# Performance work log

Measured on AMD Instinct MI355X. Metric: run time of the kernel, lower is better.

The kernel has to match this reference:

```python
import jax, jax.numpy as jnp
import numpy as np


def conv2d(x, w, b):
    pad = (w.shape[-1] - 1) // 2
    y = jax.lax.conv_general_dilated(x, w, (1, 1), [(pad, pad), (pad, pad)],
                                     dimension_numbers=('NCHW', 'OIHW', 'NCHW'))
    return y + b[None, :, None, None]


def mish(x):
    return x * jnp.tanh(jax.nn.softplus(x))


def setup_inputs() -> dict:
    key = jax.random.key(0)
    ks = jax.random.split(key, 8)
    B, C, H, W = 8, 16, 256, 256
    s = 0.1
    return dict(
        x=jax.random.normal(ks[0], (B, C, H, W), jnp.float32),
        W1=jax.random.normal(ks[1], (4, 1, 3, 3), jnp.float32) * s,      # conv1: 1->4, k=3
        b1=jnp.zeros((4,), jnp.float32),
        Wred=jax.random.normal(ks[2], (1, 4, 1, 1), jnp.float32) * s,    # involution reduce 4->1
        bred=jnp.zeros((1,), jnp.float32),
        Wspan=jax.random.normal(ks[3], (9, 1, 1, 1), jnp.float32) * s,   # involution span 1->k^2
        bspan=jnp.zeros((9,), jnp.float32),
        W2=jax.random.normal(ks[4], (C, 4 * C, 3, 3), jnp.float32) * s,  # conv2: 4C->C, k=3
        b2=jnp.zeros((C,), jnp.float32),
        Weca=jax.random.normal(ks[5], (3,), jnp.float32) * s,            # ECA 1D conv kernel
    )


def reference(x, W1, b1, Wred, bred, Wspan, bspan, W2, b2, Weca):
    B, C, H, W = x.shape
    H2 = H // 2
    K2 = 9  # 3x3 involution kernel
    # per-channel 1->4 conv + Mish: vectorize the Python channel loop by folding C into batch
    xs = x.reshape(B * C, 1, H, W)
    f = mish(conv2d(xs, W1, b1))                      # (B*C, 4, H, W)
    top, bot = f[:, :, :H2], f[:, :, H2:]             # each (B*C, 4, H2, W)
    # involution2(y1, y2): dynamic per-pixel 3x3 kernel from bottom half, applied to top half
    ker = conv2d(jax.nn.relu(conv2d(bot, Wred, bred)), Wspan, bspan)   # (B*C, 9, H2, W)
    patches = jax.lax.conv_general_dilated_patches(
        top, (3, 3), (1, 1), [(1, 1), (1, 1)],
        dimension_numbers=('NCHW', 'OIHW', 'NCHW'))                    # (B*C, 4*9, H2, W), channel-major
    patches = patches.reshape(B * C, 4, K2, H2, W)
    top_inv = (patches * ker[:, None]).sum(axis=2)                     # (B*C, 4, H2, W)
    # shuffle/concat: out channel-block i = [inv_top_i ; bottom_{(i+1) % C}] along height
    ti = top_inv.reshape(B, C, 4, H2, W)
    bo = bot.reshape(B, C, 4, H2, W)
    shuffled = jnp.concatenate([ti, jnp.roll(bo, -1, axis=1)], axis=3)  # (B, C, 4, H, W)
    shuffled = shuffled.reshape(B, 4 * C, H, W)
    out = mish(conv2d(shuffled, W2, b2))               # (B, C, H, W)
    # ECA: gate from global-avg-pooled `out`, 1D cross-correlation (k=3, pad=1) over channels
    pooled = out.mean(axis=(2, 3))                     # (B, C)
    yp = jnp.pad(pooled, ((0, 0), (1, 1)))
    gate = jax.nn.sigmoid(Weca[0] * yp[:, :-2] + Weca[1] * yp[:, 1:-1] + Weca[2] * yp[:, 2:])
    return x * gate[:, :, None, None]
```

## Files before the change

kernel.cpp:

```cpp
#include <hip/hip_runtime.h>
#include <hip/hip_bf16.h>

#define H 256
#define Wd 256
#define H2 128

typedef unsigned short ushort_t;
typedef __attribute__((ext_vector_type(8))) short short8;
typedef __attribute__((ext_vector_type(4))) float f32x4;
typedef __attribute__((ext_vector_type(2))) float f32x2;

__device__ __forceinline__ float mishf(float v){
  if (v > 15.f) return v;
  float e = __expf(v);
  float w = e*(e+2.f);
  return v * w * __builtin_amdgcn_rcpf(w + 2.f);
}

__device__ __forceinline__ ushort_t f2bf(float f){
  unsigned int u = __float_as_uint(f);
  u += 0x7fffu + ((u >> 16) & 1u);
  return (ushort_t)(u >> 16);
}
__device__ __forceinline__ float bf2f(ushort_t h){
  return __uint_as_float(((unsigned int)h) << 16);
}
__device__ __forceinline__ unsigned packbf(float a, float b){
  return (unsigned)f2bf(a) | ((unsigned)f2bf(b) << 16);
}
__device__ __forceinline__ float lo16(unsigned u){
  return __uint_as_float(u << 16);
}
__device__ __forceinline__ float hi16(unsigned u){
  return __uint_as_float(u & 0xffff0000u);
}


__global__ void k0_pack(const float* __restrict__ W2, ushort_t* __restrict__ wpack)
{
  int idx = blockIdx.x*128 + threadIdx.x;
  if (idx >= 1152) return;
  int lane  = idx & 63;
  int s     = (idx >> 6) % 9;
  int khalf = idx / 576;
  int n = lane & 15, g = lane >> 4;
  unsigned int w[4];
#pragma unroll
  for (int h = 0; h < 4; ++h){
    int ch0 = khalf*32 + g*8 + 2*h;
    unsigned lo = f2bf(W2[(n*64 + ch0  )*9 + s]);
    unsigned hi = f2bf(W2[(n*64 + ch0+1)*9 + s]);
    w[h] = lo | (hi << 16);
  }
  *(uint4*)(wpack + (size_t)idx*8) = make_uint4(w[0], w[1], w[2], w[3]);
}

__global__ __launch_bounds__(256) void k12(
    const float* __restrict__ x, const float* __restrict__ W1,
    const float* __restrict__ b1, const float* __restrict__ Wred,
    const float* __restrict__ bred, const float* __restrict__ Wspan,
    const float* __restrict__ bspan, ushort_t* __restrict__ shuf)
{
  __shared__ float xt[20][73];
  __shared__ float xb[18][73];
  __shared__ unsigned ftp[2][18][69];

  int bid = blockIdx.x;
  int n   = bid >> 5;
  int t   = bid & 31;
  int itop0 = (t >> 2) * 16;
  int j0    = (t & 3) * 64;
  int tid = threadIdx.x;
  const float* xp = x + (size_t)n * (H*Wd);

  f32x2 w01[9], w23[9], b01, b23, wspb[9];
  float wredr[4];
  float bredr = bred[0];
#pragma unroll
  for (int k=0;k<9;k++){
    w01[k] = f32x2{W1[k], W1[9+k]};
    w23[k] = f32x2{W1[18+k], W1[27+k]};
    wspb[k] = f32x2{Wspan[k], bspan[k]};
  }
  b01 = f32x2{b1[0], b1[1]};
  b23 = f32x2{b1[2], b1[3]};
#pragma unroll
  for (int m=0;m<4;m++) wredr[m] = Wred[m];

  for (int idx=tid; idx<360; idx+=256){
    int r = idx/18, q = idx - r*18;
    int grow = itop0-2+r, gcol = j0-4+q*4;
    float4 v = make_float4(0.f,0.f,0.f,0.f);
    if (grow>=0 && gcol>=0 && gcol<Wd)
      v = *(const float4*)(xp + (size_t)grow*Wd + gcol);
    int c0 = q*4;
    xt[r][c0] = v.x; xt[r][c0+1] = v.y; xt[r][c0+2] = v.z; xt[r][c0+3] = v.w;
  }
  for (int idx=tid; idx<324; idx+=256){
    int r = idx/18, q = idx - r*18;
    int grow = 127+itop0+r, gcol = j0-4+q*4;
    float4 v = make_float4(0.f,0.f,0.f,0.f);
    if (grow<H && gcol>=0 && gcol<Wd)
      v = *(const float4*)(xp + (size_t)grow*Wd + gcol);
    int c0 = q*4;
    xb[r][c0] = v.x; xb[r][c0+1] = v.y; xb[r][c0+2] = v.z; xb[r][c0+3] = v.w;
  }
  __syncthreads();

  for (int idx=tid; idx<18*66; idx+=256){
    int r = idx/66, c = idx - r*66;
    int frow = itop0-1+r, fcol = j0-1+c;
    unsigned u01 = 0u, u23 = 0u;
    if (frow>=0 && frow<H2 && fcol>=0 && fcol<Wd){
      f32x2 s01 = b01, s23 = b23;
#pragma unroll
      for (int ky=0;ky<3;ky++)
#pragma unroll
        for (int kx=0;kx<3;kx++){
          float xv = xt[r+ky][c+kx+2];
          f32x2 xv2 = f32x2{xv, xv};
          s01 = xv2*w01[ky*3+kx] + s01;
          s23 = xv2*w23[ky*3+kx] + s23;
        }
      u01 = packbf(mishf(s01.x), mishf(s01.y));
      u23 = packbf(mishf(s23.x), mishf(s23.y));
    }
    ftp[0][r][c] = u01;
    ftp[1][r][c] = u23;
  }

  int lr  = tid >> 4;
  int lc4 = (tid & 15) * 4;
  int trow = itop0 + lr;
  int bq = n >> 4, cq = n & 15;

  float fb[4][4];
  {
    float xv[3][6];
#pragma unroll
    for (int r=0;r<3;r++)
#pragma unroll
      for (int c=0;c<6;c++)
        xv[r][c] = xb[lr+r][lc4+3+c];
#pragma unroll
    for (int p=0;p<4;p++){
      f32x2 s01 = b01, s23 = b23;
#pragma unroll
      for (int ky=0;ky<3;ky++)
#pragma unroll
        for (int kx=0;kx<3;kx++){
          float v = xv[ky][p+kx];
          f32x2 v2 = f32x2{v, v};
          s01 = v2*w01[ky*3+kx] + s01;
          s23 = v2*w23[ky*3+kx] + s23;
        }
      fb[0][p] = mishf(s01.x); fb[1][p] = mishf(s01.y);
      fb[2][p] = mishf(s23.x); fb[3][p] = mishf(s23.y);
    }
  }
  int cdst = (cq + 15) & 15;
  size_t bbase = ((size_t)(bq*16 + cdst))*65536 + (size_t)(128+trow)*256 + j0 + lc4;
  {
    unsigned w0 = packbf(fb[0][0], fb[1][0]), w1 = packbf(fb[2][0], fb[3][0]);
    unsigned w2 = packbf(fb[0][1], fb[1][1]), w3 = packbf(fb[2][1], fb[3][1]);
    *(uint4*)(shuf + bbase*4) = make_uint4(w0,w1,w2,w3);
    unsigned w4 = packbf(fb[0][2], fb[1][2]), w5 = packbf(fb[2][2], fb[3][2]);
    unsigned w6 = packbf(fb[0][3], fb[1][3]), w7 = packbf(fb[2][3], fb[3][3]);
    *(uint4*)(shuf + (bbase+2)*4) = make_uint4(w4,w5,w6,w7);
  }
  float gv[4];
#pragma unroll
  for (int p=0;p<4;p++){
    float s = bredr;
#pragma unroll
    for (int m=0;m<4;m++) s = fmaf(fb[m][p], wredr[m], s);
    gv[p] = fmaxf(s, 0.f);
  }

  __syncthreads();

  unsigned fv0[3][6], fv1[3][6];
#pragma unroll
  for (int ky=0;ky<3;ky++)
#pragma unroll
    for (int c=0;c<6;c++){
      fv0[ky][c] = ftp[0][lr+ky][lc4+c];
      fv1[ky][c] = ftp[1][lr+ky][lc4+c];
    }

  float o[4][4];
#pragma unroll
  for (int p=0;p<4;p++){
    f32x2 ab0 = f32x2{0.f,0.f}, ab1 = ab0, ab2 = ab0, ab3 = ab0;
#pragma unroll
    for (int ky=0;ky<3;ky++)
#pragma unroll
      for (int kx=0;kx<3;kx++){
        f32x2 w = wspb[ky*3+kx];
        unsigned u0 = fv0[ky][p+kx], u1 = fv1[ky][p+kx];
        float a = lo16(u0), b = hi16(u0), c2 = lo16(u1), d = hi16(u1);
        ab0 = f32x2{a,a}*w + ab0;
        ab1 = f32x2{b,b}*w + ab1;
        ab2 = f32x2{c2,c2}*w + ab2;
        ab3 = f32x2{d,d}*w + ab3;
      }
    o[0][p] = fmaf(gv[p], ab0.x, ab0.y);
    o[1][p] = fmaf(gv[p], ab1.x, ab1.y);
    o[2][p] = fmaf(gv[p], ab2.x, ab2.y);
    o[3][p] = fmaf(gv[p], ab3.x, ab3.y);
  }
  size_t pbase = ((size_t)(bq*16 + cq))*65536 + (size_t)trow*256 + j0 + lc4;
  {
    unsigned w0 = packbf(o[0][0], o[1][0]), w1 = packbf(o[2][0], o[3][0]);
    unsigned w2 = packbf(o[0][1], o[1][1]), w3 = packbf(o[2][1], o[3][1]);
    *(uint4*)(shuf + pbase*4) = make_uint4(w0,w1,w2,w3);
    unsigned w4 = packbf(o[0][2], o[1][2]), w5 = packbf(o[2][2], o[3][2]);
    unsigned w6 = packbf(o[0][3], o[1][3]), w7 = packbf(o[2][3], o[3][3]);
    *(uint4*)(shuf + (pbase+2)*4) = make_uint4(w4,w5,w6,w7);
  }
}

__global__ __launch_bounds__(256) void k3_conv2(
    const ushort_t* __restrict__ shuf, const ushort_t* __restrict__ wpack,
    const float* __restrict__ b2, float* __restrict__ scratch)
{
  __shared__ f32x4 mg[2][8][64];
  __shared__ float pacc[16];

  int bid0 = blockIdx.x;
  int bid  = (bid0 & 7)*256 + (bid0 >> 3);
  int b   = bid >> 8;
  int t   = bid & 255;
  int rb  = t >> 3;
  int cb  = t & 7;
  int tid = threadIdx.x;
  int lane = tid & 63;
  int n = lane & 15;
  int g = lane >> 4;
  int wid = tid >> 6;
  int colhalf = wid & 1;
  int khalf   = wid >> 1;

  if (tid < 16) pacc[tid] = 0.f;

  const short8* wp = (const short8*)wpack + (size_t)khalf*576 + lane;
  short8 afr[9];
#pragma unroll
  for (int s = 0; s < 9; ++s) afr[s] = wp[s*64];

  f32x4 acc[8];
#pragma unroll
  for (int r = 0; r < 8; ++r) acc[r] = f32x4{0.f,0.f,0.f,0.f};

  int r0 = rb*8 - 1;
  int c  = cb*32 - 1 + colhalf*16 + n;
  int p0 = khalf*8 + g*2;
  const ushort_t* sp = shuf + ((size_t)(b*16 + p0))*262144;

#pragma unroll
  for (int hr = 0; hr < 10; ++hr){
    int grow = r0 + hr;
    bool rok = (unsigned)grow < 256u;
    uint2 va[3], vb[3];
#pragma unroll
    for (int kx = 0; kx < 3; ++kx){
      int gcol = c + kx;
      uint2 a = make_uint2(0u,0u), bv = make_uint2(0u,0u);
      if (rok && (unsigned)gcol < 256u){
        const ushort_t* pp = sp + (size_t)(grow*256 + gcol)*4;
        a  = *(const uint2*)pp;
        bv = *(const uint2*)(pp + 262144);
      }
      va[kx] = a; vb[kx] = bv;
    }
#pragma unroll
    for (int kx = 0; kx < 3; ++kx){
      union { uint4 u; short8 s; } cv;
      cv.u = make_uint4(va[kx].x, va[kx].y, vb[kx].x, vb[kx].y);
#pragma unroll
      for (int ky = 0; ky < 3; ++ky){
        int orow = hr - ky;
        if (orow >= 0 && orow < 8){
          acc[orow] = __builtin_amdgcn_mfma_f32_16x16x32_bf16(
              afr[ky*3+kx], cv.s, acc[orow], 0, 0, 0);
        }
      }
    }
  }

  if (khalf == 1){
#pragma unroll
    for (int r = 0; r < 8; ++r) mg[colhalf][r][lane] = acc[r];
  }
  __syncthreads();

  if (khalf == 0){
    float b2v[4];
#pragma unroll
    for (int q = 0; q < 4; ++q) b2v[q] = b2[g*4 + q];
    float po[4] = {0.f, 0.f, 0.f, 0.f};
#pragma unroll
    for (int r = 0; r < 8; ++r){
      f32x4 o = acc[r] + mg[colhalf][r][lane];
#pragma unroll
      for (int q = 0; q < 4; ++q) po[q] += mishf(o[q] + b2v[q]);
    }
#pragma unroll
    for (int q = 0; q < 4; ++q){
#pragma unroll
      for (int mk = 1; mk < 16; mk <<= 1) po[q] += __shfl_xor(po[q], mk);
    }
    if (n == 0){
#pragma unroll
      for (int q = 0; q < 4; ++q) atomicAdd(&pacc[g*4 + q], po[q]);
    }
  }
  __syncthreads();
  if (tid < 16) scratch[bid*16 + tid] = pacc[tid];
}

__global__ void k4_gate(const float* __restrict__ scratch,
                        const float* __restrict__ Weca,
                        float* __restrict__ gate)
{
  __shared__ float rr[16][16];
  __shared__ float pool[16];
  int b = blockIdx.x;
  int t = threadIdx.x;
  int oc = t & 15, ch = t >> 4;
  float s = 0.f;
  for (int u = 0; u < 16; ++u)
    s += scratch[(size_t)(b*256 + ch*16 + u)*16 + oc];
  rr[ch][oc] = s;
  __syncthreads();
  if (t < 16){
    float tot = 0.f;
#pragma unroll
    for (int k = 0; k < 16; ++k) tot += rr[k][t];
    pool[t] = tot * (1.0f/65536.0f);
  }
  __syncthreads();
  if (t < 16){
    float pm = (t > 0)  ? pool[t-1] : 0.f;
    float p0 = pool[t];
    float pp = (t < 15) ? pool[t+1] : 0.f;
    float z = Weca[0]*pm + Weca[1]*p0 + Weca[2]*pp;
    gate[b*16 + t] = 1.f/(1.f + __expf(-z));
  }
}

__global__ __launch_bounds__(256) void k5_scale(
    const f32x4* __restrict__ x4, const float* __restrict__ gate,
    f32x4* __restrict__ out4)
{
  int idx = blockIdx.x*256 + threadIdx.x;
  float g = gate[idx >> 14];
  f32x4 v = x4[idx] * g;
  __builtin_nontemporal_store(v, &out4[idx]);
}

extern "C" void kernel_launch(void* const* d_in, const int* in_sizes, int n_in,
                              void* d_out, int out_size, void* d_ws, size_t ws_size,
                              hipStream_t stream)
{
  const float* x     = (const float*)d_in[0];
  const float* W1    = (const float*)d_in[1];
  const float* b1    = (const float*)d_in[2];
  const float* Wred  = (const float*)d_in[3];
  const float* bred  = (const float*)d_in[4];
  const float* Wspan = (const float*)d_in[5];
  const float* bspan = (const float*)d_in[6];
  const float* W2    = (const float*)d_in[7];
  const float* b2    = (const float*)d_in[8];
  const float* Weca  = (const float*)d_in[9];

  ushort_t* shuf    = (ushort_t*)d_ws;
  float*    gate    = (float*)((char*)d_ws + 67108864);
  ushort_t* wpack   = (ushort_t*)((char*)d_ws + 67108864 + 1024);
  float*    scratch = (float*)d_out;

  k0_pack<<<9, 128, 0, stream>>>(W2, wpack);
  k12    <<<4096, 256, 0, stream>>>(x, W1, b1, Wred, bred, Wspan, bspan, shuf);
  k3_conv2<<<2048, 256, 0, stream>>>(shuf, wpack, b2, scratch);
  k4_gate<<<8, 256, 0, stream>>>(scratch, Weca, gate);
  k5_scale<<<8192, 256, 0, stream>>>((const f32x4*)x, gate, (f32x4*)d_out);
}
```

Measured before the change: 85.45 us.

## Rewrite conv1+involution kernel as register-only row stencil with packed FMA asm

The fused conv1/Mish/involution kernel drops its shared-memory tiles and barriers. Each thread now loads its input rows straight from global memory and recomputes the top-half features in registers for each of the three involution rows. The span reduction is accumulated on the fly, and inline v_pk_fma_f32 asm with op_sel broadcasts does the 4-channel conv. This removes LDS traffic and syncs and keeps the top features in fp32 instead of bf16. The cost is about three times the conv1 and Mish recompute, more global loads per thread, and higher register pressure.

```diff
diff --git a/kernel.cpp b/kernel.cpp
--- a/kernel.cpp
+++ b/kernel.cpp
@@ -28,12 +28,13 @@
 __device__ __forceinline__ unsigned packbf(float a, float b){
   return (unsigned)f2bf(a) | ((unsigned)f2bf(b) << 16);
 }
-__device__ __forceinline__ float lo16(unsigned u){
-  return __uint_as_float(u << 16);
-}
-__device__ __forceinline__ float hi16(unsigned u){
-  return __uint_as_float(u & 0xffff0000u);
-}
+
+#define PK_LO(acc, f, w) \
+  asm("v_pk_fma_f32 %0, %1, %2, %0 op_sel_hi:[1,0,1]" \
+      : "+v"(acc) : "v"(f), "s"(w))
+#define PK_HI(acc, f, w) \
+  asm("v_pk_fma_f32 %0, %1, %2, %0 op_sel:[0,1,0] op_sel_hi:[1,1,1]" \
+      : "+v"(acc) : "v"(f), "s"(w))
 
 
 __global__ void k0_pack(const float* __restrict__ W2, ushort_t* __restrict__ wpack)
@@ -55,111 +56,131 @@
   *(uint4*)(wpack + (size_t)idx*8) = make_uint4(w[0], w[1], w[2], w[3]);
 }
 
-__global__ __launch_bounds__(256) void k12(
+__global__ __launch_bounds__(256) void k12r(
     const float* __restrict__ x, const float* __restrict__ W1,
     const float* __restrict__ b1, const float* __restrict__ Wred,
     const float* __restrict__ bred, const float* __restrict__ Wspan,
     const float* __restrict__ bspan, ushort_t* __restrict__ shuf)
 {
-  __shared__ float xt[20][73];
-  __shared__ float xb[18][73];
-  __shared__ unsigned ftp[2][18][69];
-
   int bid = blockIdx.x;
   int n   = bid >> 5;
-  int t   = bid & 31;
-  int itop0 = (t >> 2) * 16;
-  int j0    = (t & 3) * 64;
+  int rg  = bid & 31;
   int tid = threadIdx.x;
+  int i   = rg*4 + (tid >> 6);
+  int j0  = (tid & 63) * 4;
   const float* xp = x + (size_t)n * (H*Wd);
-
-  f32x2 w01[9], w23[9], b01, b23, wspb[9];
-  float wredr[4];
+  bool jlo = (j0 == 0), jhi = (j0 == 252);
+
+  f32x2 w01[9], w23[9];
+  float wsp[9], bsp[9], wredr[4];
   float bredr = bred[0];
 #pragma unroll
   for (int k=0;k<9;k++){
     w01[k] = f32x2{W1[k], W1[9+k]};
     w23[k] = f32x2{W1[18+k], W1[27+k]};
-    wspb[k] = f32x2{Wspan[k], bspan[k]};
-  }
-  b01 = f32x2{b1[0], b1[1]};
-  b23 = f32x2{b1[2], b1[3]};
+    wsp[k] = Wspan[k]; bsp[k] = bspan[k];
+  }
 #pragma unroll
   for (int m=0;m<4;m++) wredr[m] = Wred[m];
-
-  for (int idx=tid; idx<360; idx+=256){
-    int r = idx/18, q = idx - r*18;
-    int grow = itop0-2+r, gcol = j0-4+q*4;
-    float4 v = make_float4(0.f,0.f,0.f,0.f);
-    if (grow>=0 && gcol>=0 && gcol<Wd)
-      v = *(const float4*)(xp + (size_t)grow*Wd + gcol);
-    int c0 = q*4;
-    xt[r][c0] = v.x; xt[r][c0+1] = v.y; xt[r][c0+2] = v.z; xt[r][c0+3] = v.w;
-  }
-  for (int idx=tid; idx<324; idx+=256){
-    int r = idx/18, q = idx - r*18;
-    int grow = 127+itop0+r, gcol = j0-4+q*4;
-    float4 v = make_float4(0.f,0.f,0.f,0.f);
-    if (grow<H && gcol>=0 && gcol<Wd)
-      v = *(const float4*)(xp + (size_t)grow*Wd + gcol);
-    int c0 = q*4;
-    xb[r][c0] = v.x; xb[r][c0+1] = v.y; xb[r][c0+2] = v.z; xb[r][c0+3] = v.w;
-  }
-  __syncthreads();
-
-  for (int idx=tid; idx<18*66; idx+=256){
-    int r = idx/66, c = idx - r*66;
-    int frow = itop0-1+r, fcol = j0-1+c;
-    unsigned u01 = 0u, u23 = 0u;
-    if (frow>=0 && frow<H2 && fcol>=0 && fcol<Wd){
-      f32x2 s01 = b01, s23 = b23;
-#pragma unroll
-      for (int ky=0;ky<3;ky++)
-#pragma unroll
-        for (int kx=0;kx<3;kx++){
-          float xv = xt[r+ky][c+kx+2];
-          f32x2 xv2 = f32x2{xv, xv};
-          s01 = xv2*w01[ky*3+kx] + s01;
-          s23 = xv2*w23[ky*3+kx] + s23;
-        }
-      u01 = packbf(mishf(s01.x), mishf(s01.y));
-      u23 = packbf(mishf(s23.x), mishf(s23.y));
-    }
-    ftp[0][r][c] = u01;
-    ftp[1][r][c] = u23;
-  }
-
-  int lr  = tid >> 4;
-  int lc4 = (tid & 15) * 4;
-  int trow = itop0 + lr;
+  f32x2 bp0 = f32x2{b1[0], b1[0]};
+  f32x2 bp1 = f32x2{b1[1], b1[1]};
+  f32x2 bp2 = f32x2{b1[2], b1[2]};
+  f32x2 bp3 = f32x2{b1[3], b1[3]};
+
+  const float4 f4z = make_float4(0.f,0.f,0.f,0.f);
+  f32x2 PA[7], PB[7], PC[7];
+
+#define LROWP(row_, P_) { \
+    int row__ = (row_); \
+    float4 lm=f4z, mm=f4z, rm=f4z; \
+    if ((unsigned)row__ < 256u){ \
+      const float* rp = xp + (size_t)row__*Wd + j0; \
+      mm = *(const float4*)rp; \
+      if (!jlo) lm = *(const float4*)(rp-4); \
+      if (!jhi) rm = *(const float4*)(rp+4); \
+    } \
+    P_[0] = f32x2{lm.z, lm.w}; \
+    P_[1] = f32x2{lm.w, mm.x}; \
+    P_[2] = f32x2{mm.x, mm.y}; \
+    P_[3] = f32x2{mm.y, mm.z}; \
+    P_[4] = f32x2{mm.z, mm.w}; \
+    P_[5] = f32x2{mm.w, rm.x}; \
+    P_[6] = f32x2{rm.x, rm.y}; \
+  }
+
+  float A[4][4], Bv[4][4];
+#pragma unroll
+  for (int m=0;m<4;m++)
+#pragma unroll
+    for (int p=0;p<4;p++){ A[m][p]=0.f; Bv[m][p]=0.f; }
+
+#define CONVSPAN(R0_, R1_, R2_, KY_) { \
+    float fm[4][6]; \
+    _Pragma("unroll") \
+    for (int cp=0; cp<3; ++cp){ \
+      f32x2 s0=bp0, s1=bp1, s2=bp2, s3=bp3; \
+      _Pragma("unroll") \
+      for (int kx=0; kx<3; ++kx){ \
+        PK_LO(s0, R0_[2*cp+kx], w01[kx]);   PK_HI(s1, R0_[2*cp+kx], w01[kx]); \
+        PK_LO(s2, R0_[2*cp+kx], w23[kx]);   PK_HI(s3, R0_[2*cp+kx], w23[kx]); \
+        PK_LO(s0, R1_[2*cp+kx], w01[3+kx]); PK_HI(s1, R1_[2*cp+kx], w01[3+kx]); \
+        PK_LO(s2, R1_[2*cp+kx], w23[3+kx]); PK_HI(s3, R1_[2*cp+kx], w23[3+kx]); \
+        PK_LO(s0, R2_[2*cp+kx], w01[6+kx]); PK_HI(s1, R2_[2*cp+kx], w01[6+kx]); \
+        PK_LO(s2, R2_[2*cp+kx], w23[6+kx]); PK_HI(s3, R2_[2*cp+kx], w23[6+kx]); \
+      } \
+      fm[0][2*cp]=mishf(s0.x); fm[0][2*cp+1]=mishf(s0.y); \
+      fm[1][2*cp]=mishf(s1.x); fm[1][2*cp+1]=mishf(s1.y); \
+      fm[2][2*cp]=mishf(s2.x); fm[2][2*cp+1]=mishf(s2.y); \
+      fm[3][2*cp]=mishf(s3.x); fm[3][2*cp+1]=mishf(s3.y); \
+    } \
+    if (jlo){ fm[0][0]=0.f; fm[1][0]=0.f; fm[2][0]=0.f; fm[3][0]=0.f; } \
+    if (jhi){ fm[0][5]=0.f; fm[1][5]=0.f; fm[2][5]=0.f; fm[3][5]=0.f; } \
+    _Pragma("unroll") \
+    for (int m=0;m<4;m++) \
+      _Pragma("unroll") \
+      for (int p=0;p<4;p++){ \
+        _Pragma("unroll") \
+        for (int kx=0;kx<3;kx++){ \
+          A[m][p]  = fmaf(fm[m][p+kx], wsp[(KY_)*3+kx], A[m][p]); \
+          Bv[m][p] = fmaf(fm[m][p+kx], bsp[(KY_)*3+kx], Bv[m][p]); \
+        } \
+      } \
+  }
+
+  LROWP(i-2, PA); LROWP(i-1, PB); LROWP(i, PC);
+  if (i >= 1) { CONVSPAN(PA, PB, PC, 0); }
+  LROWP(i+1, PA);
+  { CONVSPAN(PB, PC, PA, 1); }
+  LROWP(i+2, PB);
+  if (i <= 126) { CONVSPAN(PC, PA, PB, 2); }
+
+  LROWP(127+i, PA); LROWP(128+i, PB); LROWP(129+i, PC);
+  f32x2 sA0=bp0,sA1=bp1,sA2=bp2,sA3=bp3;
+  f32x2 sB0=bp0,sB1=bp1,sB2=bp2,sB3=bp3;
+#pragma unroll
+  for (int kx=0; kx<3; ++kx){
+    PK_LO(sA0, PA[1+kx], w01[kx]);   PK_HI(sA1, PA[1+kx], w01[kx]);
+    PK_LO(sA2, PA[1+kx], w23[kx]);   PK_HI(sA3, PA[1+kx], w23[kx]);
+    PK_LO(sB0, PA[3+kx], w01[kx]);   PK_HI(sB1, PA[3+kx], w01[kx]);
+    PK_LO(sB2, PA[3+kx], w23[kx]);   PK_HI(sB3, PA[3+kx], w23[kx]);
+    PK_LO(sA0, PB[1+kx], w01[3+kx]); PK_HI(sA1, PB[1+kx], w01[3+kx]);
+    PK_LO(sA2, PB[1+kx], w23[3+kx]); PK_HI(sA3, PB[1+kx], w23[3+kx]);
+    PK_LO(sB0, PB[3+kx], w01[3+kx]); PK_HI(sB1, PB[3+kx], w01[3+kx]);
+    PK_LO(sB2, PB[3+kx], w23[3+kx]); PK_HI(sB3, PB[3+kx], w23[3+kx]);
+    PK_LO(sA0, PC[1+kx], w01[6+kx]); PK_HI(sA1, PC[1+kx], w01[6+kx]);
+    PK_LO(sA2, PC[1+kx], w23[6+kx]); PK_HI(sA3, PC[1+kx], w23[6+kx]);
+    PK_LO(sB0, PC[3+kx], w01[6+kx]); PK_HI(sB1, PC[3+kx], w01[6+kx]);
+    PK_LO(sB2, PC[3+kx], w23[6+kx]); PK_HI(sB3, PC[3+kx], w23[6+kx]);
+  }
+  float fb[4][4];
+  fb[0][0]=mishf(sA0.x); fb[0][1]=mishf(sA0.y); fb[0][2]=mishf(sB0.x); fb[0][3]=mishf(sB0.y);
+  fb[1][0]=mishf(sA1.x); fb[1][1]=mishf(sA1.y); fb[1][2]=mishf(sB1.x); fb[1][3]=mishf(sB1.y);
+  fb[2][0]=mishf(sA2.x); fb[2][1]=mishf(sA2.y); fb[2][2]=mishf(sB2.x); fb[2][3]=mishf(sB2.y);
+  fb[3][0]=mishf(sA3.x); fb[3][1]=mishf(sA3.y); fb[3][2]=mishf(sB3.x); fb[3][3]=mishf(sB3.y);
+
   int bq = n >> 4, cq = n & 15;
-
-  float fb[4][4];
-  {
-    float xv[3][6];
-#pragma unroll
-    for (int r=0;r<3;r++)
-#pragma unroll
-      for (int c=0;c<6;c++)
-        xv[r][c] = xb[lr+r][lc4+3+c];
-#pragma unroll
-    for (int p=0;p<4;p++){
-      f32x2 s01 = b01, s23 = b23;
-#pragma unroll
-      for (int ky=0;ky<3;ky++)
-#pragma unroll
-        for (int kx=0;kx<3;kx++){
-          float v = xv[ky][p+kx];
-          f32x2 v2 = f32x2{v, v};
-          s01 = v2*w01[ky*3+kx] + s01;
-          s23 = v2*w23[ky*3+kx] + s23;
-        }
-      fb[0][p] = mishf(s01.x); fb[1][p] = mishf(s01.y);
-      fb[2][p] = mishf(s23.x); fb[3][p] = mishf(s23.y);
-    }
-  }
   int cdst = (cq + 15) & 15;
-  size_t bbase = ((size_t)(bq*16 + cdst))*65536 + (size_t)(128+trow)*256 + j0 + lc4;
+  size_t bbase = ((size_t)(bq*16 + cdst))*65536 + (size_t)(128+i)*256 + j0;
   {
     unsigned w0 = packbf(fb[0][0], fb[1][0]), w1 = packbf(fb[2][0], fb[3][0]);
     unsigned w2 = packbf(fb[0][1], fb[1][1]), w3 = packbf(fb[2][1], fb[3][1]);
@@ -177,39 +198,14 @@
     gv[p] = fmaxf(s, 0.f);
   }
 
-  __syncthreads();
-
-  unsigned fv0[3][6], fv1[3][6];
-#pragma unroll
-  for (int ky=0;ky<3;ky++)
-#pragma unroll
-    for (int c=0;c<6;c++){
-      fv0[ky][c] = ftp[0][lr+ky][lc4+c];
-      fv1[ky][c] = ftp[1][lr+ky][lc4+c];
-    }
-
   float o[4][4];
 #pragma unroll
-  for (int p=0;p<4;p++){
-    f32x2 ab0 = f32x2{0.f,0.f}, ab1 = ab0, ab2 = ab0, ab3 = ab0;
-#pragma unroll
-    for (int ky=0;ky<3;ky++)
-#pragma unroll
-      for (int kx=0;kx<3;kx++){
-        f32x2 w = wspb[ky*3+kx];
-        unsigned u0 = fv0[ky][p+kx], u1 = fv1[ky][p+kx];
-        float a = lo16(u0), b = hi16(u0), c2 = lo16(u1), d = hi16(u1);
-        ab0 = f32x2{a,a}*w + ab0;
-        ab1 = f32x2{b,b}*w + ab1;
-        ab2 = f32x2{c2,c2}*w + ab2;
-        ab3 = f32x2{d,d}*w + ab3;
-      }
-    o[0][p] = fmaf(gv[p], ab0.x, ab0.y);
-    o[1][p] = fmaf(gv[p], ab1.x, ab1.y);
-    o[2][p] = fmaf(gv[p], ab2.x, ab2.y);
-    o[3][p] = fmaf(gv[p], ab3.x, ab3.y);
-  }
-  size_t pbase = ((size_t)(bq*16 + cq))*65536 + (size_t)trow*256 + j0 + lc4;
+  for (int m=0;m<4;m++)
+#pragma unroll
+    for (int p=0;p<4;p++)
+      o[m][p] = fmaf(gv[p], A[m][p], Bv[m][p]);
+
+  size_t pbase = ((size_t)n)*65536 + (size_t)i*256 + j0;
   {
     unsigned w0 = packbf(o[0][0], o[1][0]), w1 = packbf(o[2][0], o[3][0]);
     unsigned w2 = packbf(o[0][1], o[1][1]), w3 = packbf(o[2][1], o[3][1]);
@@ -218,6 +214,8 @@
     unsigned w6 = packbf(o[0][3], o[1][3]), w7 = packbf(o[2][3], o[3][3]);
     *(uint4*)(shuf + (pbase+2)*4) = make_uint4(w4,w5,w6,w7);
   }
+#undef LROWP
+#undef CONVSPAN
 }
 
 __global__ __launch_bounds__(256) void k3_conv2(
@@ -380,7 +378,7 @@
   float*    scratch = (float*)d_out;
 
   k0_pack<<<9, 128, 0, stream>>>(W2, wpack);
-  k12    <<<4096, 256, 0, stream>>>(x, W1, b1, Wred, bred, Wspan, bspan, shuf);
+  k12r   <<<4096, 256, 0, stream>>>(x, W1, b1, Wred, bred, Wspan, bspan, shuf);
   k3_conv2<<<2048, 256, 0, stream>>>(shuf, wpack, b2, scratch);
   k4_gate<<<8, 256, 0, stream>>>(scratch, Weca, gate);
   k5_scale<<<8192, 256, 0, stream>>>((const f32x4*)x, gate, (f32x4*)d_out);
```

Measured after the change: 102.8 us. +20.3%, slower.

## Restructure conv1/involution kernel to read x directly and use packed LDS layout

Applied to the files above, without the earlier changes.

The fused conv1+mish+involution kernel no longer stages x tiles in shared memory. Each thread loads its 3x8 input window from global memory and computes 4 adjacent outputs for all 4 channels, then writes them as interleaved bf16 into a single LDS buffer read back with 16-byte vector loads. This removes a barrier and the LDS round-trip for x, and the mish overflow branch is dropped. The cost is redundant global reads, which rely on cache for reuse, plus higher register pressure. Dropping the overflow branch also risks inf/NaN from __expf on large inputs.

```diff
diff --git a/kernel.cpp b/kernel.cpp
--- a/kernel.cpp
+++ b/kernel.cpp
@@ -8,7 +8,6 @@
 typedef unsigned short ushort_t;
 typedef __attribute__((ext_vector_type(8))) short short8;
 typedef __attribute__((ext_vector_type(4))) float f32x4;
-typedef __attribute__((ext_vector_type(2))) float f32x2;
 
 __device__ __forceinline__ float mishf(float v){
   if (v > 15.f) return v;
@@ -16,14 +15,16 @@
   float w = e*(e+2.f);
   return v * w * __builtin_amdgcn_rcpf(w + 2.f);
 }
+__device__ __forceinline__ float mish_s(float v){
+  float e = __expf(v);
+  float w = e*(e+2.f);
+  return v * w * __builtin_amdgcn_rcpf(w + 2.f);
+}
 
 __device__ __forceinline__ ushort_t f2bf(float f){
   unsigned int u = __float_as_uint(f);
   u += 0x7fffu + ((u >> 16) & 1u);
   return (ushort_t)(u >> 16);
-}
-__device__ __forceinline__ float bf2f(ushort_t h){
-  return __uint_as_float(((unsigned int)h) << 16);
 }
 __device__ __forceinline__ unsigned packbf(float a, float b){
   return (unsigned)f2bf(a) | ((unsigned)f2bf(b) << 16);
@@ -55,15 +56,14 @@
   *(uint4*)(wpack + (size_t)idx*8) = make_uint4(w[0], w[1], w[2], w[3]);
 }
 
-__global__ __launch_bounds__(256) void k12(
+#define FT_STRIDE 560
+__global__ __launch_bounds__(256) void k12h(
     const float* __restrict__ x, const float* __restrict__ W1,
     const float* __restrict__ b1, const float* __restrict__ Wred,
     const float* __restrict__ bred, const float* __restrict__ Wspan,
     const float* __restrict__ bspan, ushort_t* __restrict__ shuf)
 {
-  __shared__ float xt[20][73];
-  __shared__ float xb[18][73];
-  __shared__ unsigned ftp[2][18][69];
+  __shared__ __align__(16) char ftl[18*FT_STRIDE];
 
   int bid = blockIdx.x;
   int n   = bid >> 5;
@@ -72,94 +72,106 @@
   int j0    = (t & 3) * 64;
   int tid = threadIdx.x;
   const float* xp = x + (size_t)n * (H*Wd);
-
-  f32x2 w01[9], w23[9], b01, b23, wspb[9];
-  float wredr[4];
+  const float4 f4z = make_float4(0.f,0.f,0.f,0.f);
+
+  float w1r[36], b1r[4], wsp[9], bsp[9], wredr[4];
   float bredr = bred[0];
 #pragma unroll
-  for (int k=0;k<9;k++){
-    w01[k] = f32x2{W1[k], W1[9+k]};
-    w23[k] = f32x2{W1[18+k], W1[27+k]};
-    wspb[k] = f32x2{Wspan[k], bspan[k]};
-  }
-  b01 = f32x2{b1[0], b1[1]};
-  b23 = f32x2{b1[2], b1[3]};
-#pragma unroll
-  for (int m=0;m<4;m++) wredr[m] = Wred[m];
-
-  for (int idx=tid; idx<360; idx+=256){
-    int r = idx/18, q = idx - r*18;
-    int grow = itop0-2+r, gcol = j0-4+q*4;
-    float4 v = make_float4(0.f,0.f,0.f,0.f);
-    if (grow>=0 && gcol>=0 && gcol<Wd)
-      v = *(const float4*)(xp + (size_t)grow*Wd + gcol);
-    int c0 = q*4;
-    xt[r][c0] = v.x; xt[r][c0+1] = v.y; xt[r][c0+2] = v.z; xt[r][c0+3] = v.w;
-  }
-  for (int idx=tid; idx<324; idx+=256){
-    int r = idx/18, q = idx - r*18;
-    int grow = 127+itop0+r, gcol = j0-4+q*4;
-    float4 v = make_float4(0.f,0.f,0.f,0.f);
-    if (grow<H && gcol>=0 && gcol<Wd)
-      v = *(const float4*)(xp + (size_t)grow*Wd + gcol);
-    int c0 = q*4;
-    xb[r][c0] = v.x; xb[r][c0+1] = v.y; xb[r][c0+2] = v.z; xb[r][c0+3] = v.w;
-  }
-  __syncthreads();
-
-  for (int idx=tid; idx<18*66; idx+=256){
-    int r = idx/66, c = idx - r*66;
-    int frow = itop0-1+r, fcol = j0-1+c;
-    unsigned u01 = 0u, u23 = 0u;
-    if (frow>=0 && frow<H2 && fcol>=0 && fcol<Wd){
-      f32x2 s01 = b01, s23 = b23;
-#pragma unroll
-      for (int ky=0;ky<3;ky++)
-#pragma unroll
-        for (int kx=0;kx<3;kx++){
-          float xv = xt[r+ky][c+kx+2];
-          f32x2 xv2 = f32x2{xv, xv};
-          s01 = xv2*w01[ky*3+kx] + s01;
-          s23 = xv2*w23[ky*3+kx] + s23;
+  for (int k=0;k<36;k++) w1r[k] = W1[k];
+#pragma unroll
+  for (int m=0;m<4;m++){ b1r[m] = b1[m]; wredr[m] = Wred[m]; }
+#pragma unroll
+  for (int k=0;k<9;k++){ wsp[k] = Wspan[k]; bsp[k] = bspan[k]; }
+
+#pragma unroll
+  for (int pi0 = 0; pi0 < 2; ++pi0){
+    int pi = tid + pi0*256;
+    if (pi < 306){
+      int r  = pi / 17;
+      int q  = pi - r*17;
+      int frow  = itop0 - 1 + r;
+      int fcol0 = j0 - 2 + 4*q;
+      uint4 o0 = make_uint4(0u,0u,0u,0u), o1 = make_uint4(0u,0u,0u,0u);
+      if ((unsigned)frow < 128u){
+        float v[3][8];
+        int cA = fcol0 - 2, cB = fcol0 + 2;
+#pragma unroll
+        for (int rr=0; rr<3; ++rr){
+          int xr = frow - 1 + rr;
+          bool rok = (xr >= 0);
+          const float* rp = xp + (size_t)xr*Wd;
+          float4 a = (rok && cA >= 0)   ? *(const float4*)(rp + cA) : f4z;
+          float4 b = (rok && cB <= 252) ? *(const float4*)(rp + cB) : f4z;
+          v[rr][0]=a.x; v[rr][1]=a.y; v[rr][2]=a.z; v[rr][3]=a.w;
+          v[rr][4]=b.x; v[rr][5]=b.y; v[rr][6]=b.z; v[rr][7]=b.w;
         }
-      u01 = packbf(mishf(s01.x), mishf(s01.y));
-      u23 = packbf(mishf(s23.x), mishf(s23.y));
-    }
-    ftp[0][r][c] = u01;
-    ftp[1][r][c] = u23;
+        float s[4][4];
+#pragma unroll
+        for (int m=0;m<4;m++)
+#pragma unroll
+          for (int p=0;p<4;p++) s[m][p] = b1r[m];
+#pragma unroll
+        for (int ky=0;ky<3;ky++)
+#pragma unroll
+          for (int kx=0;kx<3;kx++){
+#pragma unroll
+            for (int m=0;m<4;m++){
+              float wv = w1r[m*9+ky*3+kx];
+#pragma unroll
+              for (int p=0;p<4;p++)
+                s[m][p] = fmaf(v[ky][p+1+kx], wv, s[m][p]);
+            }
+          }
+        unsigned pw[8];
+#pragma unroll
+        for (int p=0;p<4;p++){
+          bool ok = (unsigned)(fcol0+p) < 256u;
+          pw[p*2]   = ok ? packbf(mish_s(s[0][p]), mish_s(s[1][p])) : 0u;
+          pw[p*2+1] = ok ? packbf(mish_s(s[2][p]), mish_s(s[3][p])) : 0u;
+        }
+        o0 = make_uint4(pw[0],pw[1],pw[2],pw[3]);
+        o1 = make_uint4(pw[4],pw[5],pw[6],pw[7]);
+      }
+      char* dst = ftl + r*FT_STRIDE + q*32;
+      *(uint4*)dst = o0;
+      *(uint4*)(dst+16) = o1;
+    }
   }
 
   int lr  = tid >> 4;
   int lc4 = (tid & 15) * 4;
   int trow = itop0 + lr;
   int bq = n >> 4, cq = n & 15;
-
+  int jc = j0 + lc4;
+
+  float vb[3][6];
+  bool look = (jc >= 4);
+  bool hiok = (jc <= 248);
+#pragma unroll
+  for (int rr=0; rr<3; ++rr){
+    int xr = 127 + trow + rr;
+    bool rok = (xr < 256);
+    const float* rp = xp + (size_t)xr*Wd + jc;
+    float4 m = rok ? *(const float4*)rp : f4z;
+    float lw = (rok && look) ? rp[-1] : 0.f;
+    float rw = (rok && hiok) ? rp[4]  : 0.f;
+    vb[rr][0]=lw; vb[rr][1]=m.x; vb[rr][2]=m.y; vb[rr][3]=m.z; vb[rr][4]=m.w; vb[rr][5]=rw;
+  }
   float fb[4][4];
-  {
-    float xv[3][6];
-#pragma unroll
-    for (int r=0;r<3;r++)
-#pragma unroll
-      for (int c=0;c<6;c++)
-        xv[r][c] = xb[lr+r][lc4+3+c];
+#pragma unroll
+  for (int m=0;m<4;m++)
 #pragma unroll
     for (int p=0;p<4;p++){
-      f32x2 s01 = b01, s23 = b23;
+      float s = b1r[m];
 #pragma unroll
       for (int ky=0;ky<3;ky++)
 #pragma unroll
-        for (int kx=0;kx<3;kx++){
-          float v = xv[ky][p+kx];
-          f32x2 v2 = f32x2{v, v};
-          s01 = v2*w01[ky*3+kx] + s01;
-          s23 = v2*w23[ky*3+kx] + s23;
-        }
-      fb[0][p] = mishf(s01.x); fb[1][p] = mishf(s01.y);
-      fb[2][p] = mishf(s23.x); fb[3][p] = mishf(s23.y);
-    }
-  }
+        for (int kx=0;kx<3;kx++)
+          s = fmaf(vb[ky][p+kx], w1r[m*9+ky*3+kx], s);
+      fb[m][p] = mish_s(s);
+    }
   int cdst = (cq + 15) & 15;
-  size_t bbase = ((size_t)(bq*16 + cdst))*65536 + (size_t)(128+trow)*256 + j0 + lc4;
+  size_t bbase = ((size_t)(bq*16 + cdst))*65536 + (size_t)(128+trow)*256 + jc;
   {
     unsigned w0 = packbf(fb[0][0], fb[1][0]), w1 = packbf(fb[2][0], fb[3][0]);
     unsigned w2 = packbf(fb[0][1], fb[1][1]), w3 = packbf(fb[2][1], fb[3][1]);
@@ -179,37 +191,46 @@
 
   __syncthreads();
 
-  unsigned fv0[3][6], fv1[3][6];
-#pragma unroll
-  for (int ky=0;ky<3;ky++)
-#pragma unroll
-    for (int c=0;c<6;c++){
-      fv0[ky][c] = ftp[0][lr+ky][lc4+c];
-      fv1[ky][c] = ftp[1][lr+ky][lc4+c];
-    }
+  float Aa[4][4], Bb[4][4];
+#pragma unroll
+  for (int m=0;m<4;m++)
+#pragma unroll
+    for (int p=0;p<4;p++){ Aa[m][p]=0.f; Bb[m][p]=0.f; }
+
+#pragma unroll
+  for (int ky=0;ky<3;ky++){
+    const char* src = ftl + (lr+ky)*FT_STRIDE + lc4*8;
+    float f0[8], f1[8], f2[8], f3[8];
+#pragma unroll
+    for (int jj=0;jj<4;jj++){
+      uint4 u = *(const uint4*)(src + jj*16);
+      f0[2*jj]   = lo16(u.x); f1[2*jj]   = hi16(u.x);
+      f2[2*jj]   = lo16(u.y); f3[2*jj]   = hi16(u.y);
+      f0[2*jj+1] = lo16(u.z); f1[2*jj+1] = hi16(u.z);
+      f2[2*jj+1] = lo16(u.w); f3[2*jj+1] = hi16(u.w);
+    }
+#pragma unroll
+    for (int kx=0;kx<3;kx++){
+      float ws = wsp[ky*3+kx], bs = bsp[ky*3+kx];
+#pragma unroll
+      for (int p=0;p<4;p++){
+        int ix = p + 1 + kx;
+        Aa[0][p] = fmaf(f0[ix], ws, Aa[0][p]); Bb[0][p] = fmaf(f0[ix], bs, Bb[0][p]);
+        Aa[1][p] = fmaf(f1[ix], ws, Aa[1][p]); Bb[1][p] = fmaf(f1[ix], bs, Bb[1][p]);
+        Aa[2][p] = fmaf(f2[ix], ws, Aa[2][p]); Bb[2][p] = fmaf(f2[ix], bs, Bb[2][p]);
+        Aa[3][p] = fmaf(f3[ix], ws, Aa[3][p]); Bb[3][p] = fmaf(f3[ix], bs, Bb[3][p]);
+      }
+    }
+  }
 
   float o[4][4];
 #pragma unroll
-  for (int p=0;p<4;p++){
-    f32x2 ab0 = f32x2{0.f,0.f}, ab1 = ab0, ab2 = ab0, ab3 = ab0;
-#pragma unroll
-    for (int ky=0;ky<3;ky++)
-#pragma unroll
-      for (int kx=0;kx<3;kx++){
-        f32x2 w = wspb[ky*3+kx];
-        unsigned u0 = fv0[ky][p+kx], u1 = fv1[ky][p+kx];
-        float a = lo16(u0), b = hi16(u0), c2 = lo16(u1), d = hi16(u1);
-        ab0 = f32x2{a,a}*w + ab0;
-        ab1 = f32x2{b,b}*w + ab1;
-        ab2 = f32x2{c2,c2}*w + ab2;
-        ab3 = f32x2{d,d}*w + ab3;
-      }
-    o[0][p] = fmaf(gv[p], ab0.x, ab0.y);
-    o[1][p] = fmaf(gv[p], ab1.x, ab1.y);
-    o[2][p] = fmaf(gv[p], ab2.x, ab2.y);
-    o[3][p] = fmaf(gv[p], ab3.x, ab3.y);
-  }
-  size_t pbase = ((size_t)(bq*16 + cq))*65536 + (size_t)trow*256 + j0 + lc4;
+  for (int m=0;m<4;m++)
+#pragma unroll
+    for (int p=0;p<4;p++)
+      o[m][p] = fmaf(gv[p], Aa[m][p], Bb[m][p]);
+
+  size_t pbase = ((size_t)(bq*16 + cq))*65536 + (size_t)trow*256 + jc;
   {
     unsigned w0 = packbf(o[0][0], o[1][0]), w1 = packbf(o[2][0], o[3][0]);
     unsigned w2 = packbf(o[0][1], o[1][1]), w3 = packbf(o[2][1], o[3][1]);
@@ -380,7 +401,7 @@
   float*    scratch = (float*)d_out;
 
   k0_pack<<<9, 128, 0, stream>>>(W2, wpack);
-  k12    <<<4096, 256, 0, stream>>>(x, W1, b1, Wred, bred, Wspan, bspan, shuf);
+  k12h   <<<4096, 256, 0, stream>>>(x, W1, b1, Wred, bred, Wspan, bspan, shuf);
   k3_conv2<<<2048, 256, 0, stream>>>(shuf, wpack, b2, scratch);
   k4_gate<<<8, 256, 0, stream>>>(scratch, Weca, gate);
   k5_scale<<<8192, 256, 0, stream>>>((const f32x4*)x, gate, (f32x4*)d_out);
```

After: 91.13 us. 6.6% more time.
